# Performance work log

Hardware: AMD Instinct MI355X
Metric: run time of the kernel (lower is better)

## Reference

```python
import jax, jax.numpy as jnp
import numpy as np

NUM_CLASSES = 80
TOPK = 1000
CONF_THRESH = 0.05
NMS_THRESH = 0.6
IMG = 1280.0  # input image H = W
LEVEL_N = [230400, 57600, 14400, 3600, 900]  # (1280/stride)^2 * 9 anchors, strides 8..128


def _make_boxes(k, n):
    kc, kw = jax.random.split(k)
    cxcy = jax.random.uniform(kc, (n, 2), jnp.float32, 0.0, IMG)
    wh = jax.random.uniform(kw, (n, 2), jnp.float32, 8.0, 256.0)
    x1y1 = jnp.clip(cxcy - 0.5 * wh, 0.0, IMG)
    x2y2 = jnp.clip(cxcy + 0.5 * wh, 0.0, IMG)
    return jnp.concatenate([x1y1, x2y2], axis=-1)  # [n,4] xyxy pixel coords


def setup_inputs() -> dict:
    key = jax.random.key(0)
    keys = jax.random.split(key, 10)
    inp = {}
    for i, n in enumerate(LEVEL_N):
        inp[f"cls{i}"] = jax.random.normal(keys[i], (n, NUM_CLASSES), jnp.float32) - 2.0
        inp[f"box{i}"] = _make_boxes(keys[5 + i], n)
    return inp


def _level_topk(cls_l, box_l):
    # cls_l: [N, C] logits, box_l: [N, 4]
    n = cls_l.shape[0]
    scores = jax.nn.sigmoid(cls_l).reshape(-1)           # [N*C]
    k = min(TOPK, n)
    top_scores, top_idx = jax.lax.top_k(scores, k)       # fused sort/topk per level
    labels = top_idx % NUM_CLASSES
    anchor = top_idx // NUM_CLASSES
    boxes = box_l[anchor]                                # irregular gather
    valid = top_scores > CONF_THRESH
    return top_scores, labels, boxes, valid


def _pairwise_iou(b):
    # b: [M,4] xyxy
    area = jnp.maximum(b[:, 2] - b[:, 0], 0.0) * jnp.maximum(b[:, 3] - b[:, 1], 0.0)
    lt = jnp.maximum(b[:, None, :2], b[None, :, :2])
    rb = jnp.minimum(b[:, None, 2:], b[None, :, 2:])
    wh = jnp.maximum(rb - lt, 0.0)
    inter = wh[..., 0] * wh[..., 1]
    return inter / (area[:, None] + area[None, :] - inter + 1e-9)


def _greedy_nms(boxes, scores, labels, valid):
    # class-aware greedy NMS via per-class coordinate offset trick
    m = scores.shape[0]
    s = jnp.where(valid, scores, 0.0)
    order = jnp.argsort(-s)
    boxes = boxes[order]
    s = s[order]
    labels = labels[order]
    valid = valid[order]
    offset = labels.astype(boxes.dtype)[:, None] * (IMG + 1.0)
    ious = _pairwise_iou(boxes + offset)                 # [M,M]
    idx = jnp.arange(m)

    def body(i, keep):
        sup = keep[i] & (ious[i] > NMS_THRESH) & (idx > i)
        return keep & ~sup

    keep = jax.lax.fori_loop(0, m, body, valid)
    return boxes, s, labels, keep


def reference(cls0, cls1, cls2, cls3, cls4, box0, box1, box2, box3, box4):
    cls_preds = [cls0, cls1, cls2, cls3, cls4]
    box_preds = [box0, box1, box2, box3, box4]
    parts = [_level_topk(c, b) for c, b in zip(cls_preds, box_preds)]
    scores = jnp.concatenate([p[0] for p in parts])
    labels = jnp.concatenate([p[1] for p in parts])
    boxes = jnp.concatenate([p[2] for p in parts])
    valid = jnp.concatenate([p[3] for p in parts])
    boxes, scores, labels, keep = _greedy_nms(boxes, scores, labels, valid)
    keepf = keep.astype(boxes.dtype)
    bboxes = jnp.clip(boxes / IMG, 0.0, 1.0) * keepf[:, None]  # normalize like inference_single_image
    scores = scores * keepf
    return bboxes, scores, labels, keep
```

## Files before the change

### kernel.cpp

```cpp
#include <hip/hip_runtime.h>
#include <cmath>

typedef unsigned int u32;
typedef unsigned long long u64;

#define NLEV 5
#define M_TOT 4900
#define NWORDS 77
#define CSTRIDE 80
#define CAP 65536
#define PAD_M 4928
#define NBLK 1501
#define LDSQ 1024
#define TIE_CAP 2048
#define NBLK_CMAT 3003
#define HBINS 4096
#define UCAP 128

__constant__ int   c_KLVL[5] = {1000,1000,1000,1000,900};
__constant__ int   c_LOFF[5] = {0,1000,2000,3000,4000};
__constant__ int   c_N4[5]   = {4608000,1152000,288000,72000,18000};
__constant__ int   c_BB[6]   = {0,1125,1407,1478,1496,1501};
__constant__ float c_THR[5]  = {1.0f,0.65f,0.30f,-0.15f,-0.60f};

constexpr size_t OFF_CNT   = 0;
constexpr size_t OFF_KEPT  = 256;
constexpr size_t OFF_HPRED = 1024;
constexpr size_t ZERO_BYTES= 4096;
constexpr size_t OFF_CAND  = ZERO_BYTES;
constexpr size_t OFF_KEY   = OFF_CAND + (size_t)NLEV*CAP*8;
constexpr size_t OFF_RAWB  = OFF_KEY   + (size_t)PAD_M*8;
constexpr size_t OFF_OFFB  = OFF_RAWB  + (size_t)PAD_M*16;
constexpr size_t OFF_LAB   = OFF_OFFB  + (size_t)PAD_M*16;
constexpr size_t OFF_SVAL  = OFF_LAB   + (size_t)PAD_M*4;
constexpr size_t OFF_VALID = OFF_SVAL  + (size_t)PAD_M*4;
constexpr size_t OFF_SRAWB = OFF_VALID + (size_t)PAD_M*4;
constexpr size_t OFF_SOFFB = OFF_SRAWB + (size_t)PAD_M*16;
constexpr size_t OFF_SLAB  = OFF_SOFFB + (size_t)PAD_M*16;
constexpr size_t OFF_SSVAL = OFF_SLAB  + (size_t)PAD_M*4;
constexpr size_t OFF_SVALID= OFF_SSVAL + (size_t)PAD_M*4;
constexpr size_t OFF_CMAT  = (OFF_SVALID + (size_t)PAD_M*4 + 255) & ~(size_t)255;

__device__ __forceinline__ u32 okey(u32 u){
  return (u & 0x80000000u) ? ~u : (u | 0x80000000u);
}

__device__ __forceinline__ u32 lane_prior(u64 mask){
  return __builtin_amdgcn_mbcnt_hi((u32)(mask>>32),
         __builtin_amdgcn_mbcnt_lo((u32)mask, 0u));
}

__device__ __forceinline__ u32 wave_alloc(u32* ctr, bool take){
  u64 mask = __ballot(take);
  if (mask==0ull) return 0xFFFFFFFFu;
  u32 prior = lane_prior(mask);
  u32 total = (u32)__popcll(mask);
  int leader = __ffsll((unsigned long long)mask) - 1;
  u32 base = 0;
  if (take && prior==0u) base = atomicAdd(ctr, total);
  base = __shfl(base, leader, 64);
  return take ? (base + prior) : 0xFFFFFFFFu;
}

__global__ void __launch_bounds__(256)
k_collect(const float* __restrict__ a0, const float* __restrict__ a1,
          const float* __restrict__ a2, const float* __restrict__ a3,
          const float* __restrict__ a4,
          u32* __restrict__ cnt, u32* __restrict__ cand)
{
  const int b = blockIdx.x;
  const int l = (b<c_BB[1])?0:(b<c_BB[2])?1:(b<c_BB[3])?2:(b<c_BB[4])?3:4;
  const float* __restrict__ p = (l==0)?a0:(l==1)?a1:(l==2)?a2:(l==3)?a3:a4;
  const float T = c_THR[l];
  const int n4l = c_N4[l];
  const int lb  = b - c_BB[l];
  const int base4 = lb*4096 + (int)threadIdx.x;

  __shared__ u32 lcnt, gbase;
  __shared__ u32 lbitsA[LDSQ];
  __shared__ u32 lidxA[LDSQ];
  if (threadIdx.x==0) lcnt=0u;
  __syncthreads();

  float4 xs[16];
#pragma unroll
  for (int u=0;u<16;u++){
    int q = base4 + u*256;
    int qc = (q < n4l) ? q : (n4l-1);
    xs[u] = *(const float4*)(p + (size_t)qc*4u);
  }
  u32* cdL = cand + (size_t)l*CAP*2u;
#pragma unroll
  for (int u=0;u<16;u++){
    int q = base4 + u*256;
    if (q < n4l){
      float v[4]={xs[u].x,xs[u].y,xs[u].z,xs[u].w};
#pragma unroll
      for (int i=0;i<4;i++){
        if (v[i] > T){
          u32 s = atomicAdd(&lcnt,1u);
          u32 bits = __float_as_uint(v[i]);
          u32 idx  = (u32)(q*4+i);
          if (s < LDSQ){ lbitsA[s]=bits; lidxA[s]=idx; }
          else {
            u32 pp = atomicAdd(&cnt[l],1u);
            if (pp < CAP){ u32* d=cdL+(size_t)pp*2u; d[0]=bits; d[1]=idx; }
          }
        }
      }
    }
  }
  __syncthreads();
  if (threadIdx.x==0){
    u32 m = min(lcnt,(u32)LDSQ);
    gbase = (m>0u) ? atomicAdd(&cnt[l],m) : 0xFFFFFFFFu;
  }
  __syncthreads();
  u32 m = min(lcnt,(u32)LDSQ);
  for (u32 i=threadIdx.x;i<m;i+=256u){
    u32 pp = gbase + i;
    if (pp < CAP){ u32* d=cdL+(size_t)pp*2u; d[0]=lbitsA[i]; d[1]=lidxA[i]; }
  }
}

__device__ __forceinline__ void emit_record(int l, int slot, u32 lbits, u32 idx,
    const float4* __restrict__ boxp, u64* keyA, float4* rawbA, float4* offbA,
    u32* labA, float* svalA, u32* validA)
{
#pragma clang fp contract(off)
  float x = __uint_as_float(lbits);
  float s = (float)(1.0 / (1.0 + exp(-(double)x)));
  u32 valid = (s > 0.05f) ? 1u : 0u;
  u32 label = idx % 80u;
  u32 anchor = idx / 80u;
  float4 bx = boxp[anchor];
  float off = (float)label * 1281.0f;
  float4 ob;
  ob.x = bx.x + off; ob.y = bx.y + off; ob.z = bx.z + off; ob.w = bx.w + off;
  u32 pos = ((u32)l << 25) | idx;
  u32 khi = valid ? okey(lbits) : 0u;
  int g = c_LOFF[l] + slot;
  keyA[g]  = ((u64)khi << 32) | (u64)(u32)(~pos);
  rawbA[g] = bx; offbA[g] = ob; labA[g] = label;
  svalA[g] = valid ? s : 0.0f; validA[g] = valid;
}

__device__ __forceinline__ void emit_dummy(int l, int slot,
    u64* keyA, float4* rawbA, float4* offbA, u32* labA, float* svalA, u32* validA)
{
  u32 pos = ((u32)l<<25) | (0x1FFFFFFu - (u32)slot);
  int g = c_LOFF[l]+slot;
  float4 z; z.x=z.y=z.z=z.w=0.0f;
  keyA[g]=(u64)(u32)(~pos);
  rawbA[g]=z; offbA[g]=z; labA[g]=0u; svalA[g]=0.0f; validA[g]=0u;
}

__global__ void __launch_bounds__(1024)
k_select(u32* __restrict__ cnt, u32* __restrict__ cand,
         const float* __restrict__ a0, const float* __restrict__ a1,
         const float* __restrict__ a2, const float* __restrict__ a3,
         const float* __restrict__ a4,
         const float4* b0, const float4* b1, const float4* b2,
         const float4* b3, const float4* b4,
         u64* keyA, float4* rawbA, float4* offbA,
         u32* labA, float* svalA, u32* validA)
{
  const int l = blockIdx.x;
  const float4* boxp = (l==0)?b0:(l==1)?b1:(l==2)?b2:(l==3)?b3:b4;
  const float* __restrict__ p = (l==0)?a0:(l==1)?a1:(l==2)?a2:(l==3)?a3:a4;
  u32* cdL = cand + (size_t)l*CAP*2u;
  const u32* cd = cdL;
  const int k = c_KLVL[l];
  u32 count = min(cnt[l], (u32)CAP);

  __shared__ u32 lhist[4][HBINS];
  __shared__ u32 sufw[16];
  __shared__ u32 c0_s, kk_s, cnt_s;
  __shared__ u32 emit_s, ntie_s;
  __shared__ u32 tb[TIE_CAP], ti[TIE_CAP];

  const u32 tid = threadIdx.x;
  const u32 lane = tid & 63u;
  const u32 wave = tid >> 6;
  if (tid==0){ emit_s=0u; ntie_s=0u; c0_s=0u; kk_s=0u; }
  for (u32 i=tid;i<4u*HBINS;i+=1024u) ((u32*)lhist)[i]=0u;
  __syncthreads();

  if (count < (u32)k){
    const int nElem = c_N4[l]*4;
    float Tprev = c_THR[l];
    for (int r=1; r<=7 && count<(u32)k; r++){
      float Tn = (r<7) ? (c_THR[l] - 1.5f*(float)r) : -3.0e38f;
      for (u32 i=tid; i<(u32)nElem; i+=1024u){
        float x = p[i];
        if (x>Tn && x<=Tprev){
          u32 pp = atomicAdd(&cnt[l],1u);
          if (pp<CAP){ u32* d=cdL+(size_t)pp*2u; d[0]=__float_as_uint(x); d[1]=i; }
        }
      }
      __syncthreads();
      if (tid==0) cnt_s = atomicAdd(&cnt[l],0u);
      __syncthreads();
      count = min(cnt_s,(u32)CAP);
      Tprev = Tn;
    }
  }

  if (count > (u32)k){
    const u32 rep = wave & 3u;
    for (u32 i=tid;i<count;i+=1024u)
      atomicAdd(&lhist[rep][okey(cd[2*(size_t)i])>>20], 1u);
    __syncthreads();
    u32 base = tid*4u;
    u32 hb[4]; u32 ls=0u;
#pragma unroll
    for (int b2_=0;b2_<4;b2_++){
      u32 h = lhist[0][base+(u32)b2_]+lhist[1][base+(u32)b2_]
            + lhist[2][base+(u32)b2_]+lhist[3][base+(u32)b2_];
      hb[b2_]=h; ls+=h;
    }
    u32 x = ls;
#pragma unroll
    for (int off=1; off<64; off<<=1){
      u32 y = __shfl_down(x, off, 64);
      if (lane + (u32)off < 64u) x += y;
    }
    if (lane==0u) sufw[wave]=x;
    __syncthreads();
    u32 wsuf=0u;
    for (u32 w=wave+1u;w<16u;w++) wsuf += sufw[w];
    u32 suffix_after = wsuf + (x - ls);
    if (suffix_after < (u32)k && (u32)k <= suffix_after + ls){
      u32 run = suffix_after;
      for (int b2_=3;b2_>=0;b2_--){
        u32 h = hb[b2_];
        run += h;
        if (run >= (u32)k){ c0_s = base+(u32)b2_; kk_s = (u32)k - (run - h); break; }
      }
    }
    __syncthreads();
    const u32 c0 = c0_s, kk = kk_s;

    u32 iters = (count + 1023u)/1024u;
    for (u32 it=0; it<iters; it++){
      u32 i = it*1024u + tid;
      bool in = i < count;
      u32 bits = in ? cd[2*(size_t)i] : 0u;
      u32 idx  = in ? cd[2*(size_t)i+1] : 0u;
      u32 h    = okey(bits)>>20;
      bool hi  = in && (h > c0);
      bool tie = in && (h == c0);
      u32 s = wave_alloc(&emit_s, hi);
      if (hi && s < (u32)k)
        emit_record(l,(int)s,bits,idx,boxp,keyA,rawbA,offbA,labA,svalA,validA);
      u32 t = wave_alloc(&ntie_s, tie);
      if (tie && t < (u32)TIE_CAP){ tb[t]=bits; ti[t]=idx; }
    }
    __syncthreads();

    u32 nt = min(ntie_s,(u32)TIE_CAP);
    for (u32 e=tid;e<nt;e+=1024u){
      u32 mk = okey(tb[e]); u32 mi = ti[e];
      u32 r=0u;
      for (u32 e2=0;e2<nt;e2++){
        u32 k2 = okey(tb[e2]);
        r += (k2>mk || (k2==mk && ti[e2]<mi)) ? 1u : 0u;
      }
      if (r < kk){
        u32 s = atomicAdd(&emit_s,1u);
        if (s < (u32)k)
          emit_record(l,(int)s,tb[e],mi,boxp,keyA,rawbA,offbA,labA,svalA,validA);
      }
    }
  } else {
    u32 iters = (count + 1023u)/1024u;
    for (u32 it=0; it<iters; it++){
      u32 i = it*1024u + tid;
      bool in = i < count;
      u32 bits = in ? cd[2*(size_t)i] : 0u;
      u32 idx  = in ? cd[2*(size_t)i+1] : 0u;
      u32 s = wave_alloc(&emit_s, in);
      if (in && s < (u32)k)
        emit_record(l,(int)s,bits,idx,boxp,keyA,rawbA,offbA,labA,svalA,validA);
    }
  }
  __syncthreads();
  u32 em = min(emit_s,(u32)k);
  for (u32 i=em+tid;i<(u32)k;i+=1024u)
    emit_dummy(l,(int)i,keyA,rawbA,offbA,labA,svalA,validA);
}

__global__ void __launch_bounds__(256)
k_rank(const u64* __restrict__ keyA,
       const float4* __restrict__ rawbA, const float4* __restrict__ offbA,
       const u32* __restrict__ labA, const float* __restrict__ svalA,
       const u32* __restrict__ validA,
       float4* srawb, float4* soffb, u32* slab, float* ssval, u32* svalid)
{
  __shared__ u64 sk[M_TOT];
  __shared__ u32 part[3][64];
  for (int i=threadIdx.x;i<M_TOT;i+=256) sk[i]=keyA[i];
  __syncthreads();
  int lane = threadIdx.x & 63;
  int wave = threadIdx.x >> 6;
  int i = blockIdx.x*64 + lane;
  u64 mk = sk[(i<M_TOT)?i:0];
  int j0 = wave*1225;
  u32 r=0;
#pragma unroll 5
  for (int j=j0;j<j0+1225;j++) r += (sk[j]>mk)?1u:0u;
  if (wave) part[wave-1][lane]=r;
  __syncthreads();
  if (wave==0 && i<M_TOT){
    r += part[0][lane]+part[1][lane]+part[2][lane];
    srawb[r]=rawbA[i]; soffb[r]=offbA[i]; slab[r]=labA[i];
    ssval[r]=svalA[i]; svalid[r]=validA[i];
  }
}

__global__ void __launch_bounds__(256)
k_cmat(const float4* __restrict__ soffb, u64* __restrict__ cmat,
       u64* __restrict__ haspred)
{
#pragma clang fp contract(off)
  int bi = blockIdx.x;
  int jt = (int)((sqrtf(8.0f*(float)bi+1.0f)-1.0f)*0.5f);
  while ((jt+1)*(jt+2)/2 <= bi) jt++;
  while (jt*(jt+1)/2 > bi) jt--;
  int wt = bi - jt*(jt+1)/2;

  __shared__ float rx[64],ry[64],rz[64],rw[64],ra[64];
  __shared__ float cx[64],cy[64],cz[64],cw[64],cae[64];
  int tid = threadIdx.x;
  if (tid<64){
    float4 b = soffb[wt*64+tid];
    rx[tid]=b.x; ry[tid]=b.y; rz[tid]=b.z; rw[tid]=b.w;
    ra[tid]=fmaxf(b.z-b.x,0.0f)*fmaxf(b.w-b.y,0.0f);
  } else if (tid<128){
    int c=tid-64;
    float4 b = soffb[jt*64+c];
    cx[c]=b.x; cy[c]=b.y; cz[c]=b.z; cw[c]=b.w;
    cae[c]=fmaxf(b.z-b.x,0.0f)*fmaxf(b.w-b.y,0.0f);
  }
  __syncthreads();
  int lane = tid & 63;
  int wave = tid >> 6;
  int rowg = wt*64 + lane;
  float bx=rx[lane], by=ry[lane], bz=rz[lane], bw=rw[lane], bar=ra[lane];
  for (int cc=wave*16; cc<wave*16+16; cc++){
    int jg = jt*64 + cc;
    if (jg >= M_TOT) continue;
    float jx=cx[cc], jy=cy[cc], jz=cz[cc], jw=cw[cc], jar=cae[cc];
    float ltx=fmaxf(bx,jx), lty=fmaxf(by,jy);
    float rbx=fminf(bz,jz), rby=fminf(bw,jw);
    float wx=fmaxf(rbx-ltx,0.0f), wy=fmaxf(rby-lty,0.0f);
    float inter=wx*wy;
    float iou = inter/(bar+jar-inter+1e-9f);
    bool bit = (rowg < jg) && (iou > 0.6f);
    u64 word = __ballot(bit);
    if (lane==0){
      cmat[(size_t)jg*CSTRIDE + (size_t)wt] = word;
      if (word) atomicOr(&haspred[jg>>6], 1ull<<(jg&63));
    }
  }
}

__global__ void __launch_bounds__(256)
k_resolve(const u64* __restrict__ cmat, const u32* __restrict__ svalid,
          const u64* __restrict__ haspred, u64* __restrict__ kept)
{
  __shared__ u64 k0[NWORDS];
  __shared__ u64 uw[NWORDS];
  __shared__ u32 ubase[NWORDS];
  __shared__ unsigned short ulist[UCAP];
  __shared__ u64 pmask[UCAP][2];
  __shared__ u32 dhit[UCAP];
  __shared__ u32 nu_s;
  const u32 tid=threadIdx.x, lane=tid&63u, wave=tid>>6;

  for (u32 w=wave; w<NWORDS; w+=4){
    int j = (int)(w*64u+lane);
    u32 sv = (j<M_TOT)? svalid[j] : 0u;
    u64 hp = haspred[w];
    bool hpb = (hp>>lane)&1ull;
    u64 keepb = __ballot(sv && !hpb);
    u64 undb  = __ballot(sv && hpb);
    if (lane==0){ k0[w]=keepb; uw[w]=undb; }
  }
  __syncthreads();
  if (tid==0){
    u32 n=0;
    for (int w=0;w<NWORDS;w++){
      ubase[w]=n;
      u64 U=uw[w];
      while(U){ int b=__builtin_ctzll(U); U&=U-1ull;
                if (n<UCAP) ulist[n]=(unsigned short)(w*64+b); n++; }
    }
    nu_s=n;
  }
  __syncthreads();
  u32 nu = nu_s;

  if (nu>0u && nu<=UCAP){
    for (u32 t=tid; t<nu; t+=256u){
      u32 j = (u32)ulist[t];
      const u64* row = cmat + (size_t)j*CSTRIDE;
      u32 wmax = j>>6;
      u64 hit=0ull, pm0=0ull, pm1=0ull;
      for (u32 w=0; w<=wmax; w++){
        u64 rw = row[w];
        hit |= rw & k0[w];
        u64 ub = rw & uw[w];
        while(ub){
          int b=__builtin_ctzll(ub); ub&=ub-1ull;
          u32 idx = ubase[w] + (u32)__popcll(uw[w] & ((b==0)?0ull:((1ull<<b)-1ull)));
          if (idx<64u) pm0 |= 1ull<<idx; else pm1 |= 1ull<<(idx-64u);
        }
      }
      dhit[t] = (hit!=0ull)?1u:0u;
      pmask[t][0]=pm0; pmask[t][1]=pm1;
    }
    __syncthreads();
    if (tid==0){
      u64 ku0=0ull, ku1=0ull;
      for (u32 t=0;t<nu;t++){
        bool sup = dhit[t] || ((pmask[t][0]&ku0)|(pmask[t][1]&ku1))!=0ull;
        if (!sup){
          if (t<64u) ku0|=1ull<<t; else ku1|=1ull<<(t-64u);
          u32 j=(u32)ulist[t];
          k0[j>>6] |= 1ull<<(j&63u);
        }
      }
    }
    __syncthreads();
  } else if (nu>UCAP){
    if (tid==0){
      for (int w=0;w<NWORDS;w++){
        u64 U=uw[w];
        while(U){
          int b=__builtin_ctzll(U); U&=U-1ull;
          u32 j=(u32)(w*64+b);
          const u64* row = cmat + (size_t)j*CSTRIDE;
          u64 hit=0ull; u32 wmax=j>>6;
          for (u32 w2=0;w2<=wmax;w2++) hit |= row[w2] & k0[w2];
          if (hit==0ull) k0[j>>6] |= 1ull<<(j&63u);
        }
      }
    }
    __syncthreads();
  }
  for (u32 w=tid; w<NWORDS; w+=256u) kept[w]=k0[w];
}

__global__ void k_out(const u64* __restrict__ kept, const float4* __restrict__ srawb,
                      const float* __restrict__ ssval, const u32* __restrict__ slab,
                      float* __restrict__ out)
{
  int t=blockIdx.x*blockDim.x+threadIdx.x;
  if (t<M_TOT){
    u32 kb=(u32)((kept[t>>6]>>(t&63))&1ull);
    float kf=kb?1.0f:0.0f;
    float4 b=srawb[t];
    out[4*t+0]=fminf(fmaxf(b.x/1280.0f,0.0f),1.0f)*kf;
    out[4*t+1]=fminf(fmaxf(b.y/1280.0f,0.0f),1.0f)*kf;
    out[4*t+2]=fminf(fmaxf(b.z/1280.0f,0.0f),1.0f)*kf;
    out[4*t+3]=fminf(fmaxf(b.w/1280.0f,0.0f),1.0f)*kf;
    out[19600+t]=ssval[t]*kf;
    out[24500+t]=(float)slab[t];
    out[29400+t]=kf;
  }
}

extern "C" void kernel_launch(void* const* d_in, const int* in_sizes, int n_in,
                              void* d_out, int out_size, void* d_ws, size_t ws_size,
                              hipStream_t stream)
{
  const float* cls[5]={nullptr,nullptr,nullptr,nullptr,nullptr};
  const float* box[5]={nullptr,nullptr,nullptr,nullptr,nullptr};
  static const int clsEl[5]={18432000,4608000,1152000,288000,72000};
  static const int boxEl[5]={921600,230400,57600,14400,3600};
  for (int i=0;i<n_in;i++){
    int sz=in_sizes[i];
    bool done=false;
    for (int l=0;l<5 && !done;l++){
      if (sz==clsEl[l] && !cls[l]){ cls[l]=(const float*)d_in[i]; done=true; }
      else if (sz==boxEl[l] && !box[l]){ box[l]=(const float*)d_in[i]; done=true; }
    }
  }
  unsigned char* ws=(unsigned char*)d_ws;
  u32* cnt   = (u32*)(ws+OFF_CNT);
  u64* kept  = (u64*)(ws+OFF_KEPT);
  u64* hpred = (u64*)(ws+OFF_HPRED);
  u32* cand  = (u32*)(ws+OFF_CAND);
  u64* keyA  = (u64*)(ws+OFF_KEY);
  float4* rawbA=(float4*)(ws+OFF_RAWB);
  float4* offbA=(float4*)(ws+OFF_OFFB);
  u32* labA  = (u32*)(ws+OFF_LAB);
  float* svalA=(float*)(ws+OFF_SVAL);
  u32* validA=(u32*)(ws+OFF_VALID);
  float4* srawb=(float4*)(ws+OFF_SRAWB);
  float4* soffb=(float4*)(ws+OFF_SOFFB);
  u32* slab  = (u32*)(ws+OFF_SLAB);
  float* ssval=(float*)(ws+OFF_SSVAL);
  u32* svalid=(u32*)(ws+OFF_SVALID);
  u64* cmat  = (u64*)(ws+OFF_CMAT);
  float* out = (float*)d_out;

  hipMemsetAsync(ws, 0, ZERO_BYTES, stream);

  k_collect<<<dim3(NBLK),dim3(256),0,stream>>>(cls[0],cls[1],cls[2],cls[3],cls[4],cnt,cand);

  k_select<<<dim3(5),dim3(1024),0,stream>>>(cnt,cand,
      cls[0],cls[1],cls[2],cls[3],cls[4],
      (const float4*)box[0],(const float4*)box[1],(const float4*)box[2],
      (const float4*)box[3],(const float4*)box[4],
      keyA,rawbA,offbA,labA,svalA,validA);

  k_rank  <<<dim3(77),dim3(256),0,stream>>>(keyA,rawbA,offbA,labA,svalA,validA,
                                            srawb,soffb,slab,ssval,svalid);
  k_cmat  <<<dim3(NBLK_CMAT),dim3(256),0,stream>>>(soffb,cmat,hpred);
  k_resolve<<<dim3(1),dim3(256),0,stream>>>(cmat,svalid,hpred,kept);
  k_out   <<<dim3(20),dim3(256),0,stream>>>(kept,srawb,ssval,slab,out);
}
```

Measured before the change: 290.9 us.

## Shard candidate buffers per level and bin histogram by linear score

Candidate collection now goes into 32 per-level shards, each with its own counter, plus an overflow region, instead of one global counter per level. This spreads atomic contention on the level counter across shards. The select histogram now bins by a linear quantization of the logit above the threshold instead of the top bits of the ordered key. The aim is finer bins and fewer ties at the top-k boundary. In exchange, select must loop over 33 regions, and a slow global-memory fallback rank path was added for when ties overflow the shared tie buffer.

```diff
diff --git a/kernel.cpp b/kernel.cpp
--- a/kernel.cpp
+++ b/kernel.cpp
@@ -8,10 +8,13 @@
 #define M_TOT 4900
 #define NWORDS 77
 #define CSTRIDE 80
-#define CAP 65536
 #define PAD_M 4928
 #define NBLK 1501
-#define LDSQ 1024
+#define LDSQ 2048
+#define NSH 32
+#define SHCAP 2048
+#define OVCAP 16384
+#define LVST (NSH*SHCAP + OVCAP)
 #define TIE_CAP 2048
 #define NBLK_CMAT 3003
 #define HBINS 4096
@@ -24,11 +27,12 @@
 __constant__ float c_THR[5]  = {1.0f,0.65f,0.30f,-0.15f,-0.60f};
 
 constexpr size_t OFF_CNT   = 0;
-constexpr size_t OFF_KEPT  = 256;
-constexpr size_t OFF_HPRED = 1024;
+constexpr size_t OFF_OCNT  = 768;
+constexpr size_t OFF_KEPT  = 1024;
+constexpr size_t OFF_HPRED = 2048;
 constexpr size_t ZERO_BYTES= 4096;
-constexpr size_t OFF_CAND  = ZERO_BYTES;
-constexpr size_t OFF_KEY   = OFF_CAND + (size_t)NLEV*CAP*8;
+constexpr size_t OFF_CAND  = 4096;
+constexpr size_t OFF_KEY   = OFF_CAND + (size_t)NLEV*LVST*8;
 constexpr size_t OFF_RAWB  = OFF_KEY   + (size_t)PAD_M*8;
 constexpr size_t OFF_OFFB  = OFF_RAWB  + (size_t)PAD_M*16;
 constexpr size_t OFF_LAB   = OFF_OFFB  + (size_t)PAD_M*16;
@@ -45,6 +49,12 @@
   return (u & 0x80000000u) ? ~u : (u | 0x80000000u);
 }
 
+__device__ __forceinline__ u32 qbin(u32 bits, float T){
+  float x = __uint_as_float(bits);
+  int b = (int)((x - T)*800.0f);
+  return (u32)max(0, min(HBINS-1, b));
+}
+
 __device__ __forceinline__ u32 lane_prior(u64 mask){
   return __builtin_amdgcn_mbcnt_hi((u32)(mask>>32),
          __builtin_amdgcn_mbcnt_lo((u32)mask, 0u));
@@ -66,7 +76,7 @@
 k_collect(const float* __restrict__ a0, const float* __restrict__ a1,
           const float* __restrict__ a2, const float* __restrict__ a3,
           const float* __restrict__ a4,
-          u32* __restrict__ cnt, u32* __restrict__ cand)
+          u32* __restrict__ cnt, u32* __restrict__ ocnt, u32* __restrict__ cand)
 {
   const int b = blockIdx.x;
   const int l = (b<c_BB[1])?0:(b<c_BB[2])?1:(b<c_BB[3])?2:(b<c_BB[4])?3:4;
@@ -74,6 +84,7 @@
   const float T = c_THR[l];
   const int n4l = c_N4[l];
   const int lb  = b - c_BB[l];
+  const int shard = lb & (NSH-1);
   const int base4 = lb*4096 + (int)threadIdx.x;
 
   __shared__ u32 lcnt, gbase;
@@ -89,7 +100,8 @@
     int qc = (q < n4l) ? q : (n4l-1);
     xs[u] = *(const float4*)(p + (size_t)qc*4u);
   }
-  u32* cdL = cand + (size_t)l*CAP*2u;
+  u32* cdS = cand + ((size_t)l*LVST + (size_t)shard*SHCAP)*2u;
+  u32* cdO = cand + ((size_t)l*LVST + (size_t)NSH*SHCAP)*2u;
 #pragma unroll
   for (int u=0;u<16;u++){
     int q = base4 + u*256;
@@ -103,8 +115,8 @@
           u32 idx  = (u32)(q*4+i);
           if (s < LDSQ){ lbitsA[s]=bits; lidxA[s]=idx; }
           else {
-            u32 pp = atomicAdd(&cnt[l],1u);
-            if (pp < CAP){ u32* d=cdL+(size_t)pp*2u; d[0]=bits; d[1]=idx; }
+            u32 pp = atomicAdd(&ocnt[l],1u);
+            if (pp < OVCAP){ u32* d=cdO+(size_t)pp*2u; d[0]=bits; d[1]=idx; }
           }
         }
       }
@@ -113,13 +125,17 @@
   __syncthreads();
   if (threadIdx.x==0){
     u32 m = min(lcnt,(u32)LDSQ);
-    gbase = (m>0u) ? atomicAdd(&cnt[l],m) : 0xFFFFFFFFu;
+    gbase = (m>0u) ? atomicAdd(&cnt[l*NSH+shard],m) : 0xFFFFFFFFu;
   }
   __syncthreads();
   u32 m = min(lcnt,(u32)LDSQ);
   for (u32 i=threadIdx.x;i<m;i+=256u){
     u32 pp = gbase + i;
-    if (pp < CAP){ u32* d=cdL+(size_t)pp*2u; d[0]=lbitsA[i]; d[1]=lidxA[i]; }
+    if (pp < SHCAP){ u32* d=cdS+(size_t)pp*2u; d[0]=lbitsA[i]; d[1]=lidxA[i]; }
+    else {
+      u32 q = atomicAdd(&ocnt[l],1u);
+      if (q < OVCAP){ u32* d=cdO+(size_t)q*2u; d[0]=lbitsA[i]; d[1]=lidxA[i]; }
+    }
   }
 }
 
@@ -156,7 +172,7 @@
 }
 
 __global__ void __launch_bounds__(1024)
-k_select(u32* __restrict__ cnt, u32* __restrict__ cand,
+k_select(u32* __restrict__ cnt, u32* __restrict__ ocnt, u32* __restrict__ cand,
          const float* __restrict__ a0, const float* __restrict__ a1,
          const float* __restrict__ a2, const float* __restrict__ a3,
          const float* __restrict__ a4,
@@ -168,14 +184,16 @@
   const int l = blockIdx.x;
   const float4* boxp = (l==0)?b0:(l==1)?b1:(l==2)?b2:(l==3)?b3:b4;
   const float* __restrict__ p = (l==0)?a0:(l==1)?a1:(l==2)?a2:(l==3)?a3:a4;
-  u32* cdL = cand + (size_t)l*CAP*2u;
-  const u32* cd = cdL;
+  const float Tl = c_THR[l];
+  u32* lvbase = cand + (size_t)l*LVST*2u;
+  u32* cdO = lvbase + (size_t)NSH*SHCAP*2u;
   const int k = c_KLVL[l];
-  u32 count = min(cnt[l], (u32)CAP);
 
   __shared__ u32 lhist[4][HBINS];
   __shared__ u32 sufw[16];
-  __shared__ u32 c0_s, kk_s, cnt_s;
+  __shared__ u32 rlen[NSH+1];
+  __shared__ u32 count_s;
+  __shared__ u32 c0_s, kk_s;
   __shared__ u32 emit_s, ntie_s;
   __shared__ u32 tb[TIE_CAP], ti[TIE_CAP];
 
@@ -183,33 +201,45 @@
   const u32 lane = tid & 63u;
   const u32 wave = tid >> 6;
   if (tid==0){ emit_s=0u; ntie_s=0u; c0_s=0u; kk_s=0u; }
+  if (tid<NSH) rlen[tid]=min(cnt[l*NSH+tid],(u32)SHCAP);
+  if (tid==NSH) rlen[NSH]=min(ocnt[l],(u32)OVCAP);
   for (u32 i=tid;i<4u*HBINS;i+=1024u) ((u32*)lhist)[i]=0u;
   __syncthreads();
+  if (tid==0){ u32 c=0; for(int r=0;r<=NSH;r++) c+=rlen[r]; count_s=c; }
+  __syncthreads();
+  u32 count = count_s;
 
   if (count < (u32)k){
     const int nElem = c_N4[l]*4;
-    float Tprev = c_THR[l];
+    float Tprev = Tl;
     for (int r=1; r<=7 && count<(u32)k; r++){
-      float Tn = (r<7) ? (c_THR[l] - 1.5f*(float)r) : -3.0e38f;
+      float Tn = (r<7) ? (Tl - 1.5f*(float)r) : -3.0e38f;
       for (u32 i=tid; i<(u32)nElem; i+=1024u){
         float x = p[i];
         if (x>Tn && x<=Tprev){
-          u32 pp = atomicAdd(&cnt[l],1u);
-          if (pp<CAP){ u32* d=cdL+(size_t)pp*2u; d[0]=__float_as_uint(x); d[1]=i; }
+          u32 pp = atomicAdd(&ocnt[l],1u);
+          if (pp<OVCAP){ u32* d=cdO+(size_t)pp*2u; d[0]=__float_as_uint(x); d[1]=i; }
         }
       }
       __syncthreads();
-      if (tid==0) cnt_s = atomicAdd(&cnt[l],0u);
+      if (tid==0){
+        rlen[NSH]=min(atomicAdd(&ocnt[l],0u),(u32)OVCAP);
+        u32 c=0; for(int rr=0;rr<=NSH;rr++) c+=rlen[rr]; count_s=c;
+      }
       __syncthreads();
-      count = min(cnt_s,(u32)CAP);
+      count = count_s;
       Tprev = Tn;
     }
   }
 
   if (count > (u32)k){
     const u32 rep = wave & 3u;
-    for (u32 i=tid;i<count;i+=1024u)
-      atomicAdd(&lhist[rep][okey(cd[2*(size_t)i])>>20], 1u);
+    for (int r=0;r<=NSH;r++){
+      const u32* cdR = lvbase + ((r<NSH)?(size_t)r*SHCAP:(size_t)NSH*SHCAP)*2u;
+      u32 len = rlen[r];
+      for (u32 i=tid;i<len;i+=1024u)
+        atomicAdd(&lhist[rep][qbin(cdR[2*(size_t)i],Tl)], 1u);
+    }
     __syncthreads();
     u32 base = tid*4u;
     u32 hb[4]; u32 ls=0u;
@@ -241,47 +271,82 @@
     __syncthreads();
     const u32 c0 = c0_s, kk = kk_s;
 
-    u32 iters = (count + 1023u)/1024u;
-    for (u32 it=0; it<iters; it++){
-      u32 i = it*1024u + tid;
-      bool in = i < count;
-      u32 bits = in ? cd[2*(size_t)i] : 0u;
-      u32 idx  = in ? cd[2*(size_t)i+1] : 0u;
-      u32 h    = okey(bits)>>20;
-      bool hi  = in && (h > c0);
-      bool tie = in && (h == c0);
-      u32 s = wave_alloc(&emit_s, hi);
-      if (hi && s < (u32)k)
-        emit_record(l,(int)s,bits,idx,boxp,keyA,rawbA,offbA,labA,svalA,validA);
-      u32 t = wave_alloc(&ntie_s, tie);
-      if (tie && t < (u32)TIE_CAP){ tb[t]=bits; ti[t]=idx; }
-    }
-    __syncthreads();
-
-    u32 nt = min(ntie_s,(u32)TIE_CAP);
-    for (u32 e=tid;e<nt;e+=1024u){
-      u32 mk = okey(tb[e]); u32 mi = ti[e];
-      u32 r=0u;
-      for (u32 e2=0;e2<nt;e2++){
-        u32 k2 = okey(tb[e2]);
-        r += (k2>mk || (k2==mk && ti[e2]<mi)) ? 1u : 0u;
-      }
-      if (r < kk){
-        u32 s = atomicAdd(&emit_s,1u);
-        if (s < (u32)k)
-          emit_record(l,(int)s,tb[e],mi,boxp,keyA,rawbA,offbA,labA,svalA,validA);
+    for (int r=0;r<=NSH;r++){
+      const u32* cdR = lvbase + ((r<NSH)?(size_t)r*SHCAP:(size_t)NSH*SHCAP)*2u;
+      u32 len = rlen[r];
+      u32 iters = (len + 1023u)/1024u;
+      for (u32 it=0; it<iters; it++){
+        u32 i = it*1024u + tid;
+        bool in = i < len;
+        u32 bits = in ? cdR[2*(size_t)i] : 0u;
+        u32 idx  = in ? cdR[2*(size_t)i+1] : 0u;
+        u32 h    = qbin(bits,Tl);
+        bool hi  = in && (h > c0);
+        bool tie = in && (h == c0);
+        u32 s = wave_alloc(&emit_s, hi);
+        if (hi && s < (u32)k)
+          emit_record(l,(int)s,bits,idx,boxp,keyA,rawbA,offbA,labA,svalA,validA);
+        u32 t = wave_alloc(&ntie_s, tie);
+        if (tie && t < (u32)TIE_CAP){ tb[t]=bits; ti[t]=idx; }
+      }
+    }
+    __syncthreads();
+
+    u32 nt = ntie_s;
+    if (nt <= (u32)TIE_CAP){
+      for (u32 e=tid;e<nt;e+=1024u){
+        u32 mk = okey(tb[e]); u32 mi = ti[e];
+        u32 r=0u;
+        for (u32 e2=0;e2<nt;e2++){
+          u32 k2 = okey(tb[e2]);
+          r += (k2>mk || (k2==mk && ti[e2]<mi)) ? 1u : 0u;
+        }
+        if (r < kk){
+          u32 s = atomicAdd(&emit_s,1u);
+          if (s < (u32)k)
+            emit_record(l,(int)s,tb[e],mi,boxp,keyA,rawbA,offbA,labA,svalA,validA);
+        }
+      }
+    } else {
+      for (int r=0;r<=NSH;r++){
+        const u32* cdR = lvbase + ((r<NSH)?(size_t)r*SHCAP:(size_t)NSH*SHCAP)*2u;
+        u32 len = rlen[r];
+        for (u32 i=tid;i<len;i+=1024u){
+          u32 bits=cdR[2*(size_t)i], idx=cdR[2*(size_t)i+1];
+          if (qbin(bits,Tl)!=c0) continue;
+          u32 mk=okey(bits); u32 rank=0u;
+          for (int r2=0;r2<=NSH;r2++){
+            const u32* c2 = lvbase + ((r2<NSH)?(size_t)r2*SHCAP:(size_t)NSH*SHCAP)*2u;
+            u32 len2 = rlen[r2];
+            for (u32 j=0;j<len2;j++){
+              u32 b2=c2[2*(size_t)j];
+              if (qbin(b2,Tl)!=c0) continue;
+              u32 k2=okey(b2);
+              rank += (k2>mk || (k2==mk && c2[2*(size_t)j+1]<idx)) ? 1u : 0u;
+            }
+          }
+          if (rank<kk){
+            u32 s=atomicAdd(&emit_s,1u);
+            if (s<(u32)k)
+              emit_record(l,(int)s,bits,idx,boxp,keyA,rawbA,offbA,labA,svalA,validA);
+          }
+        }
       }
     }
   } else {
-    u32 iters = (count + 1023u)/1024u;
-    for (u32 it=0; it<iters; it++){
-      u32 i = it*1024u + tid;
-      bool in = i < count;
-      u32 bits = in ? cd[2*(size_t)i] : 0u;
-      u32 idx  = in ? cd[2*(size_t)i+1] : 0u;
-      u32 s = wave_alloc(&emit_s, in);
-      if (in && s < (u32)k)
-        emit_record(l,(int)s,bits,idx,boxp,keyA,rawbA,offbA,labA,svalA,validA);
+    for (int r=0;r<=NSH;r++){
+      const u32* cdR = lvbase + ((r<NSH)?(size_t)r*SHCAP:(size_t)NSH*SHCAP)*2u;
+      u32 len = rlen[r];
+      u32 iters = (len + 1023u)/1024u;
+      for (u32 it=0; it<iters; it++){
+        u32 i = it*1024u + tid;
+        bool in = i < len;
+        u32 bits = in ? cdR[2*(size_t)i] : 0u;
+        u32 idx  = in ? cdR[2*(size_t)i+1] : 0u;
+        u32 s = wave_alloc(&emit_s, in);
+        if (in && s < (u32)k)
+          emit_record(l,(int)s,bits,idx,boxp,keyA,rawbA,offbA,labA,svalA,validA);
+      }
     }
   }
   __syncthreads();
@@ -489,6 +554,7 @@
   }
   unsigned char* ws=(unsigned char*)d_ws;
   u32* cnt   = (u32*)(ws+OFF_CNT);
+  u32* ocnt  = (u32*)(ws+OFF_OCNT);
   u64* kept  = (u64*)(ws+OFF_KEPT);
   u64* hpred = (u64*)(ws+OFF_HPRED);
   u32* cand  = (u32*)(ws+OFF_CAND);
@@ -508,9 +574,9 @@
 
   hipMemsetAsync(ws, 0, ZERO_BYTES, stream);
 
-  k_collect<<<dim3(NBLK),dim3(256),0,stream>>>(cls[0],cls[1],cls[2],cls[3],cls[4],cnt,cand);
-
-  k_select<<<dim3(5),dim3(1024),0,stream>>>(cnt,cand,
+  k_collect<<<dim3(NBLK),dim3(256),0,stream>>>(cls[0],cls[1],cls[2],cls[3],cls[4],cnt,ocnt,cand);
+
+  k_select<<<dim3(5),dim3(1024),0,stream>>>(cnt,ocnt,cand,
       cls[0],cls[1],cls[2],cls[3],cls[4],
       (const float4*)box[0],(const float4*)box[1],(const float4*)box[2],
       (const float4*)box[3],(const float4*)box[4],
```

New measurement: 285.4 us. Within noise of the previous version (-1.9%).
